# Optimization experiments

Measured on AMD Instinct MI355X. Metric: run time of the kernel, lower is better.

## Reference

```python
import jax, jax.numpy as jnp
import numpy as np

EPS = 1e-5  # BatchNorm2d default eps (eval mode with running stats)


def _bn(v, params):
    # params: [4, C] = (gamma, beta, running_mean, running_var); channel on last axis of v
    g, b, m, var = params[0], params[1], params[2], params[3]
    return (v - m) * jax.lax.rsqrt(var + EPS) * g + b


def _gather(feat, idx):
    # feat: [B, N, C], idx: [B, M, K] -> [B, M, K, C]
    B, M, K = idx.shape
    flat = jnp.take_along_axis(feat, idx.reshape(B, M * K, 1), axis=1)
    return flat.reshape(B, M, K, feat.shape[-1])


def xconv_forward(p, x, q, w1, bn1, w2, bn2, wt1, bnt1, wt2, bnt2, wt3, wc, bno):
    selu = jax.nn.selu
    B = p.shape[0]
    K = wt1.shape[2]  # kernel_size
    pT = jnp.transpose(p, (0, 2, 1))  # [B, N, 3]
    # KNN: squared distances [B, M, N], take K nearest (dilation=1)
    d2 = (jnp.sum(q * q, axis=-1, keepdims=True)
          + jnp.sum(pT * pT, axis=-1)[:, None, :]
          - 2.0 * jnp.einsum('bmc,bnc->bmn', q, pT))
    _, idx = jax.lax.top_k(-d2, K)  # [B, M, K]
    p_nb = _gather(pT, idx)                     # [B, M, K, 3]
    p_hat = p_nb - q[:, :, None, :]             # [B, M, K, 3]
    # mlp1: two 1x1 conv + BN + SELU stacks on p_hat
    h = selu(_bn(jnp.einsum('bmkc,dc->bmkd', p_hat, w1), bn1))
    h = selu(_bn(jnp.einsum('bmkd,ed->bmke', h, w2), bn2))  # [B, M, K, mid]
    # gather input features and concat
    xT = jnp.transpose(x, (0, 2, 1))            # [B, N, Cin]
    x_nb = _gather(xT, idx)                     # [B, M, K, Cin]
    x_hat = jnp.concatenate([h, x_nb], axis=-1)  # [B, M, K, mid+Cin]
    # mlp2: X-transform matrix T (conv [1,K] contracts the neighbor axis)
    t = selu(_bn(jnp.einsum('bmkc,ock->bmo', p_hat, wt1), bnt1))  # [B, M, K^2]
    t = selu(_bn(jnp.einsum('bmo,po->bmp', t, wt2), bnt2))
    t = jnp.einsum('bmp,qp->bmq', t, wt3)
    M = q.shape[1]
    T = t.reshape(B, M, K, K)                   # matches torch view(B,K,K,M).permute(0,3,1,2)
    y = jnp.matmul(T, x_hat)                    # [B, M, K, mid+Cin]
    # final conv [1,K] + BN + SELU -> [B, out, M]
    y = jnp.einsum('bmkc,ock->bmo', y, wc)
    y = selu(_bn(y, bno))
    return jnp.transpose(q, (0, 2, 1)), jnp.transpose(y, (0, 2, 1))


def _bn_pack(key, c):
    k1, k2, k3, k4 = jax.random.split(key, 4)
    gamma = 1.0 + 0.1 * jax.random.normal(k1, (c,), jnp.float32)
    beta = 0.1 * jax.random.normal(k2, (c,), jnp.float32)
    mean = 0.1 * jax.random.normal(k3, (c,), jnp.float32)
    var = jax.random.uniform(k4, (c,), jnp.float32, 0.5, 1.5)
    return jnp.stack([gamma, beta, mean, var], axis=0)


def setup_inputs() -> dict:
    B, N, M, K, CIN, COUT = 4, 8192, 2048, 16, 64, 256
    MID, K2 = COUT // 4, K * K
    key = jax.random.key(0)
    ks = jax.random.split(key, 16)
    return {
        'p': jax.random.normal(ks[0], (B, 3, N), jnp.float32),
        'x': jax.random.normal(ks[1], (B, CIN, N), jnp.float32),
        'q': jax.random.normal(ks[2], (B, M, 3), jnp.float32),
        'w1': 0.1 * jax.random.normal(ks[3], (MID, 3), jnp.float32),
        'bn1': _bn_pack(ks[4], MID),
        'w2': 0.1 * jax.random.normal(ks[5], (MID, MID), jnp.float32),
        'bn2': _bn_pack(ks[6], MID),
        'wt1': 0.1 * jax.random.normal(ks[7], (K2, 3, K), jnp.float32),
        'bnt1': _bn_pack(ks[8], K2),
        'wt2': 0.05 * jax.random.normal(ks[9], (K2, K2), jnp.float32),
        'bnt2': _bn_pack(ks[10], K2),
        'wt3': 0.05 * jax.random.normal(ks[11], (K2, K2), jnp.float32),
        'wc': 0.05 * jax.random.normal(ks[12], (COUT, MID + CIN, K), jnp.float32),
        'bno': _bn_pack(ks[13], COUT),
    }


def reference(p, x, q, w1, bn1, w2, bn2, wt1, bnt1, wt2, bnt2, wt3, wc, bno):
    return xconv_forward(p, x, q, w1, bn1, w2, bn2, wt1, bnt1, wt2, bnt2, wt3, wc, bno)
```

## Files before the change

### kernel.cpp

```cpp
#include <hip/hip_runtime.h>
#include <hip/hip_bf16.h>
#include <float.h>

#define NPTS 8192
#define KNB  16
#define CINC 64
#define MIDC 64
#define EPSBN 1e-5f

typedef unsigned short u16;
typedef u16   us8   __attribute__((ext_vector_type(8)));
typedef __bf16 bf16x8 __attribute__((ext_vector_type(8)));
typedef float  f32x4  __attribute__((ext_vector_type(4)));

__device__ __forceinline__ float selu_f(float x) {
    const float sc = 1.0507009873554805f;
    const float al = 1.6732632423543772f;
    return x > 0.f ? sc * x : sc * al * expm1f(x);
}
__device__ __forceinline__ float bn_f(float v, const float* __restrict__ bnp, int C, int c) {
    float g = bnp[c], b = bnp[C + c], mu = bnp[2 * C + c], va = bnp[3 * C + c];
    return (v - mu) * (1.0f / sqrtf(va + EPSBN)) * g + b;
}
__device__ __forceinline__ u16 f2bf(float v) {
    __hip_bfloat16 h = __float2bfloat16(v);
    return *reinterpret_cast<u16*>(&h);
}

__device__ __forceinline__ unsigned long long wavemin_u64(unsigned long long h) {
#pragma unroll
    for (int s = 32; s >= 1; s >>= 1) {
        const unsigned int ohi = __shfl_xor((unsigned int)(h >> 32), s);
        const unsigned int olo = __shfl_xor((unsigned int)(h & 0xFFFFFFFFu), s);
        const unsigned long long o = ((unsigned long long)ohi << 32) | olo;
        if (o < h) h = o;
    }
    return h;
}

__global__ __launch_bounds__(256) void knn_kernel(const float* __restrict__ p,
                                                  const float* __restrict__ q,
                                                  int* __restrict__ idx_out,
                                                  float* __restrict__ phat) {
    const int w = threadIdx.x >> 6, lane = threadIdx.x & 63;
    const int bm = blockIdx.x * 4 + w;
    const int b = bm >> 11;
    const float qx = q[bm * 3 + 0], qy = q[bm * 3 + 1], qz = q[bm * 3 + 2];
    const float qq = __fadd_rn(__fadd_rn(__fmul_rn(qx, qx), __fmul_rn(qy, qy)), __fmul_rn(qz, qz));
    const float* px = p + (size_t)b * 3 * NPTS;
    const float* py = px + NPTS;
    const float* pz = py + NPTS;

    unsigned long long mn = ~0ull;
#pragma unroll 2
    for (int j = 0; j < NPTS / 64; ++j) {
        const int n = lane + j * 64;
        const float ax = px[n], ay = py[n], az = pz[n];
        const float pp = __fadd_rn(__fadd_rn(__fmul_rn(ax, ax), __fmul_rn(ay, ay)), __fmul_rn(az, az));
        const float dt = __fmaf_rn(az, qz, __fmaf_rn(ay, qy, __fmul_rn(ax, qx)));
        const float d2 = __fsub_rn(__fadd_rn(qq, pp), __fmul_rn(2.0f, dt));
        const unsigned int bits = __float_as_uint(d2);
        const unsigned int key = bits ^ ((unsigned int)((int)bits >> 31) | 0x80000000u);
        const unsigned long long nk = ((unsigned long long)key << 32) | (unsigned int)n;
        if (nk < mn) mn = nk;
    }
    unsigned long long T;
    {
        unsigned long long mcur = mn;
        for (int r = 0; r < 16; ++r) {
            const unsigned long long h = wavemin_u64(mcur);
            if (r == 15) T = h;
            if (mcur == h) mcur = ~0ull;
        }
    }

    unsigned long long K[16];
#pragma unroll
    for (int i = 0; i < 16; ++i) K[i] = ~0ull;

#pragma unroll 2
    for (int j = 0; j < NPTS / 64; ++j) {
        const int n = lane + j * 64;
        const float ax = px[n], ay = py[n], az = pz[n];
        const float pp = __fadd_rn(__fadd_rn(__fmul_rn(ax, ax), __fmul_rn(ay, ay)), __fmul_rn(az, az));
        const float dt = __fmaf_rn(az, qz, __fmaf_rn(ay, qy, __fmul_rn(ax, qx)));
        const float d2 = __fsub_rn(__fadd_rn(qq, pp), __fmul_rn(2.0f, dt));
        const unsigned int bits = __float_as_uint(d2);
        const unsigned int key = bits ^ ((unsigned int)((int)bits >> 31) | 0x80000000u);
        const unsigned long long nk = ((unsigned long long)key << 32) | (unsigned int)n;
        if (__any(nk <= T)) {
            if (nk <= T && nk < K[15]) {
                bool c[16];
#pragma unroll
                for (int i = 0; i < 16; ++i) c[i] = nk < K[i];
#pragma unroll
                for (int i = 15; i >= 1; --i) K[i] = c[i] ? (c[i - 1] ? K[i - 1] : nk) : K[i];
                K[0] = c[0] ? nk : K[0];
            }
        }
    }

    unsigned long long win_i = 0, win_p = 0;
    for (int r = 0; r < 16; ++r) {
        const unsigned long long h = wavemin_u64(K[0]);
        const bool own = (K[0] == h);
#pragma unroll
        for (int i = 0; i < 15; ++i) K[i] = own ? K[i + 1] : K[i];
        K[15] = own ? ~0ull : K[15];
        if (r == lane) win_i = h;
        if (lane < 48 && r == (lane / 3)) win_p = h;
    }
    if (lane < 16) idx_out[bm * 16 + lane] = (int)(win_i & 0xFFFFFFFFu);
    if (lane < 48) {
        const int kk = lane / 3, c = lane - kk * 3;
        const int n = (int)(win_p & 0xFFFFFFFFu);
        phat[(size_t)bm * 48 + lane] = p[((size_t)b * 3 + c) * NPTS + n] - q[bm * 3 + c];
    }
}

__global__ __launch_bounds__(256) void mlp1_kernel(const float* __restrict__ x,
                                                   const float* __restrict__ w1,
                                                   const float* __restrict__ bn1,
                                                   const float* __restrict__ w2,
                                                   const float* __restrict__ bn2,
                                                   const int* __restrict__ idxb,
                                                   const float* __restrict__ phat,
                                                   float* __restrict__ xhat) {
    __shared__ float ph[48];
    __shared__ float h1[16 * 64];
    __shared__ float4 w2s4[16][64];
    __shared__ int idxs[16];
    const int bm = blockIdx.x;
    const int b = bm >> 11;
    const int t = threadIdx.x;
    if (t < 48) ph[t] = phat[(size_t)bm * 48 + t];
    if (t < 16) idxs[t] = idxb[bm * 16 + t];
#pragma unroll
    for (int i = 0; i < 4; ++i) {
        const int fi = t + i * 256;
        const int e = fi >> 4, dq = fi & 15;
        w2s4[dq][e] = ((const float4*)w2)[fi];
    }
    __syncthreads();
#pragma unroll
    for (int i = 0; i < 4; ++i) {
        const int o = t + i * 256;
        const int kk = o >> 6, d = o & 63;
        float s = ph[kk * 3 + 0] * w1[d * 3 + 0] + ph[kk * 3 + 1] * w1[d * 3 + 1] + ph[kk * 3 + 2] * w1[d * 3 + 2];
        h1[kk * 64 + d] = selu_f(bn_f(s, bn1, MIDC, d));
    }
    __syncthreads();
#pragma unroll
    for (int i = 0; i < 4; ++i) {
        const int o = t + i * 256;
        const int kk = o >> 6, e = o & 63;
        const float4* h4 = (const float4*)&h1[kk * 64];
        float s = 0.f;
#pragma unroll
        for (int dq = 0; dq < 16; ++dq) {
            const float4 hv = h4[dq];
            const float4 wv = w2s4[dq][e];
            s += hv.x * wv.x; s += hv.y * wv.y; s += hv.z * wv.z; s += hv.w * wv.w;
        }
        xhat[(size_t)bm * 2048 + kk * 128 + e] = selu_f(bn_f(s, bn2, MIDC, e));
    }
#pragma unroll
    for (int i = 0; i < 4; ++i) {
        const int o = t + i * 256;
        const int kk = o >> 6, c = o & 63;
        xhat[(size_t)bm * 2048 + kk * 128 + 64 + c] = x[((size_t)b * CINC + c) * NPTS + idxs[kk]];
    }
}

template <int MODE>
__global__ __launch_bounds__(256) void gemm_bt(const float* __restrict__ A, int lda,
                                               const float* __restrict__ B, int ldb,
                                               float* __restrict__ C, int ldc,
                                               int Kd, const float* __restrict__ bnp, int Nc) {
    __shared__ float As[16][68];
    __shared__ float Bs[16][68];
    const int t = threadIdx.x;
    const int tx = t & 15, ty = t >> 4;
    const int row0 = blockIdx.y * 64, col0 = blockIdx.x * 64;
    const int r = t >> 2, q4 = t & 3;
    float acc[4][4] = {};
    for (int k0 = 0; k0 < Kd; k0 += 16) {
        const float4 av = *(const float4*)(A + (size_t)(row0 + r) * lda + k0 + q4 * 4);
        const float4 bv = *(const float4*)(B + (size_t)(col0 + r) * ldb + k0 + q4 * 4);
        As[q4 * 4 + 0][r] = av.x; As[q4 * 4 + 1][r] = av.y;
        As[q4 * 4 + 2][r] = av.z; As[q4 * 4 + 3][r] = av.w;
        Bs[q4 * 4 + 0][r] = bv.x; Bs[q4 * 4 + 1][r] = bv.y;
        Bs[q4 * 4 + 2][r] = bv.z; Bs[q4 * 4 + 3][r] = bv.w;
        __syncthreads();
#pragma unroll
        for (int kk = 0; kk < 16; ++kk) {
            float a0 = As[kk][ty * 4 + 0], a1 = As[kk][ty * 4 + 1];
            float a2 = As[kk][ty * 4 + 2], a3 = As[kk][ty * 4 + 3];
            float b0 = Bs[kk][tx * 4 + 0], b1 = Bs[kk][tx * 4 + 1];
            float b2 = Bs[kk][tx * 4 + 2], b3 = Bs[kk][tx * 4 + 3];
            acc[0][0] += a0 * b0; acc[0][1] += a0 * b1; acc[0][2] += a0 * b2; acc[0][3] += a0 * b3;
            acc[1][0] += a1 * b0; acc[1][1] += a1 * b1; acc[1][2] += a1 * b2; acc[1][3] += a1 * b3;
            acc[2][0] += a2 * b0; acc[2][1] += a2 * b1; acc[2][2] += a2 * b2; acc[2][3] += a2 * b3;
            acc[3][0] += a3 * b0; acc[3][1] += a3 * b1; acc[3][2] += a3 * b2; acc[3][3] += a3 * b3;
        }
        __syncthreads();
    }
#pragma unroll
    for (int i = 0; i < 4; ++i) {
#pragma unroll
        for (int j = 0; j < 4; ++j) {
            const int row = row0 + ty * 4 + i, col = col0 + tx * 4 + j;
            float v = acc[i][j];
            if (MODE >= 1) v = selu_f(bn_f(v, bnp, Nc, col));
            if (MODE == 2) {
                C[(((size_t)(row >> 11)) * Nc + col) * 2048 + (row & 2047)] = v;
            } else {
                C[(size_t)row * ldc + col] = v;
            }
        }
    }
}

template <int EMIT_BF>
__global__ __launch_bounds__(256) void xtrans_kernel(float* __restrict__ xhat,
                                                     const float* __restrict__ tmat,
                                                     u16* __restrict__ xhb) {
    __shared__ float xs[2048];
    __shared__ float Tm[256];
    const int bm = blockIdx.x, t = threadIdx.x;
#pragma unroll
    for (int i = 0; i < 8; ++i) xs[t + i * 256] = xhat[(size_t)bm * 2048 + t + i * 256];
    Tm[t] = tmat[(size_t)bm * 256 + t];
    __syncthreads();
    float y[8];
#pragma unroll
    for (int i = 0; i < 8; ++i) {
        const int o = t + i * 256, kk = o >> 7, c = o & 127;
        float s = 0.f;
#pragma unroll
        for (int j = 0; j < 16; ++j) s += Tm[kk * 16 + j] * xs[j * 128 + c];
        y[i] = s;
    }
    if (EMIT_BF) {
#pragma unroll
        for (int i = 0; i < 8; ++i) xhb[(size_t)bm * 2048 + t + i * 256] = f2bf(y[i]);
    } else {
#pragma unroll
        for (int i = 0; i < 8; ++i) xhat[(size_t)bm * 2048 + t + i * 256] = y[i];
    }
}

__global__ __launch_bounds__(256) void gemm_mfma_final(const u16* __restrict__ XHB,
                                                       const u16* __restrict__ WCBH,
                                                       const float* __restrict__ bno,
                                                       float* __restrict__ out1) {
    __shared__ u16 As[64][72];
    __shared__ u16 Bs[64][72];
    const int t = threadIdx.x;
    const int w = t >> 6, lane = t & 63;
    const int wm = w >> 1, wn = w & 1;
    const int row0 = blockIdx.y * 64, col0 = blockIdx.x * 64;
    const int srow = t >> 2, skq = t & 3;

    f32x4 acc[2][2] = {};

    for (int k0 = 0; k0 < 2048; k0 += 64) {
        __syncthreads();
        const u16* ga = XHB + (size_t)(row0 + srow) * 2048 + k0 + skq * 16;
        const u16* gb = WCBH + (size_t)(col0 + srow) * 2048 + k0 + skq * 16;
        *(us8*)&As[srow][skq * 16 + 0] = *(const us8*)(ga + 0);
        *(us8*)&As[srow][skq * 16 + 8] = *(const us8*)(ga + 8);
        *(us8*)&Bs[srow][skq * 16 + 0] = *(const us8*)(gb + 0);
        *(us8*)&Bs[srow][skq * 16 + 8] = *(const us8*)(gb + 8);
        __syncthreads();
#pragma unroll
        for (int ks = 0; ks < 2; ++ks) {
            const int kb = ks * 32 + (lane >> 4) * 8;
            const bf16x8 a0 = *(const bf16x8*)&As[wm * 32 + (lane & 15)][kb];
            const bf16x8 a1 = *(const bf16x8*)&As[wm * 32 + 16 + (lane & 15)][kb];
            const bf16x8 b0 = *(const bf16x8*)&Bs[wn * 32 + (lane & 15)][kb];
            const bf16x8 b1 = *(const bf16x8*)&Bs[wn * 32 + 16 + (lane & 15)][kb];
            acc[0][0] = __builtin_amdgcn_mfma_f32_16x16x32_bf16(a0, b0, acc[0][0], 0, 0, 0);
            acc[0][1] = __builtin_amdgcn_mfma_f32_16x16x32_bf16(a0, b1, acc[0][1], 0, 0, 0);
            acc[1][0] = __builtin_amdgcn_mfma_f32_16x16x32_bf16(a1, b0, acc[1][0], 0, 0, 0);
            acc[1][1] = __builtin_amdgcn_mfma_f32_16x16x32_bf16(a1, b1, acc[1][1], 0, 0, 0);
        }
    }
#pragma unroll
    for (int mi = 0; mi < 2; ++mi) {
#pragma unroll
        for (int ni = 0; ni < 2; ++ni) {
            const int col = col0 + wn * 32 + ni * 16 + (lane & 15);
            const int rowg = row0 + wm * 32 + mi * 16 + (lane >> 4) * 4;
            const int b = rowg >> 11, m = rowg & 2047;
            float4 v;
            v.x = selu_f(bn_f(acc[mi][ni][0], bno, 256, col));
            v.y = selu_f(bn_f(acc[mi][ni][1], bno, 256, col));
            v.z = selu_f(bn_f(acc[mi][ni][2], bno, 256, col));
            v.w = selu_f(bn_f(acc[mi][ni][3], bno, 256, col));
            *(float4*)(out1 + ((size_t)(b * 256 + col)) * 2048 + m) = v;
        }
    }
}

__global__ void transpose_q_kernel(const float* __restrict__ q, float* __restrict__ out0) {
    const int t = blockIdx.x * 256 + threadIdx.x;
    if (t >= 4 * 3 * 2048) return;
    const int b = t / 6144, rem = t % 6144, c = rem >> 11, m = rem & 2047;
    out0[t] = q[((size_t)b * 2048 + m) * 3 + c];
}
__global__ void prep_wt1_kernel(const float* __restrict__ wt1, float* __restrict__ wt1r) {
    const int t = blockIdx.x * 256 + threadIdx.x;
    if (t >= 256 * 48) return;
    const int o = t / 48, rem = t % 48, kk = rem / 3, c = rem % 3;
    wt1r[t] = wt1[o * 48 + c * 16 + kk];
}
__global__ void prep_wc_kernel(const float* __restrict__ wc, float* __restrict__ wcb) {
    const int t = blockIdx.x * 256 + threadIdx.x;
    if (t >= 256 * 2048) return;
    const int o = t >> 11, f = t & 2047, kk = f >> 7, c = f & 127;
    wcb[t] = wc[o * 2048 + c * 16 + kk];
}
__global__ void prep_wcbh_kernel(const float* __restrict__ wcb, u16* __restrict__ wcbh) {
    const int t = blockIdx.x * 256 + threadIdx.x;
    if (t >= 256 * 2048) return;
    wcbh[t] = f2bf(wcb[t]);
}

extern "C" void kernel_launch(void* const* d_in, const int* in_sizes, int n_in,
                              void* d_out, int out_size, void* d_ws, size_t ws_size,
                              hipStream_t stream) {
    const float* p    = (const float*)d_in[0];
    const float* x    = (const float*)d_in[1];
    const float* q    = (const float*)d_in[2];
    const float* w1   = (const float*)d_in[3];
    const float* bn1  = (const float*)d_in[4];
    const float* w2   = (const float*)d_in[5];
    const float* bn2  = (const float*)d_in[6];
    const float* wt1  = (const float*)d_in[7];
    const float* bnt1 = (const float*)d_in[8];
    const float* wt2  = (const float*)d_in[9];
    const float* bnt2 = (const float*)d_in[10];
    const float* wt3  = (const float*)d_in[11];
    const float* wc   = (const float*)d_in[12];
    const float* bno  = (const float*)d_in[13];
    float* out = (float*)d_out;

    float* ws   = (float*)d_ws;
    float* WT1R = ws;
    float* WCB  = WT1R + 12288;
    int*   IDX  = (int*)(WCB + 524288);
    float* PHAT = (float*)(IDX + 131072);
    float* BUFA = PHAT + 393216;
    float* BUFB = BUFA + 2097152;
    float* XHAT = BUFB + 2097152;
    u16*   XHB  = (u16*)(XHAT + 16777216);
    u16*   WCBH = XHB + 16777216;
    const size_t NEED = (22032384ull + 8388608ull + 262144ull) * 4ull;
    const bool use_mfma = (ws_size >= NEED);

    transpose_q_kernel<<<96, 256, 0, stream>>>(q, out);
    prep_wt1_kernel<<<48, 256, 0, stream>>>(wt1, WT1R);
    prep_wc_kernel<<<2048, 256, 0, stream>>>(wc, WCB);
    if (use_mfma) prep_wcbh_kernel<<<2048, 256, 0, stream>>>(WCB, WCBH);

    knn_kernel<<<2048, 256, 0, stream>>>(p, q, IDX, PHAT);
    mlp1_kernel<<<8192, 256, 0, stream>>>(x, w1, bn1, w2, bn2, IDX, PHAT, XHAT);

    gemm_bt<1><<<dim3(4, 128), 256, 0, stream>>>(PHAT, 48, WT1R, 48, BUFA, 256, 48, bnt1, 256);
    gemm_bt<1><<<dim3(4, 128), 256, 0, stream>>>(BUFA, 256, wt2, 256, BUFB, 256, 256, bnt2, 256);
    gemm_bt<0><<<dim3(4, 128), 256, 0, stream>>>(BUFB, 256, wt3, 256, BUFA, 256, 256, nullptr, 256);

    if (use_mfma) {
        xtrans_kernel<1><<<8192, 256, 0, stream>>>(XHAT, BUFA, XHB);
        gemm_mfma_final<<<dim3(4, 128), 256, 0, stream>>>(XHB, WCBH, bno, out + 24576);
    } else {
        xtrans_kernel<0><<<8192, 256, 0, stream>>>(XHAT, BUFA, nullptr);
        gemm_bt<2><<<dim3(4, 128), 256, 0, stream>>>(XHAT, 2048, WCB, 2048, out + 24576, 0, 2048, bno, 256);
    }
}
```

Before: 292.4 us.

## Pre-transpose x to point-major and vectorize neighbor gather and X-transform

Adds a tiled transpose kernel that writes x as [B,N,C] into scratch (reusing BUFA before the T-matrix GEMMs overwrite it). The mlp1 neighbor gather then reads contiguous float4 rows per neighbor instead of 64 strided scalar loads, which removes uncoalesced gathers. The xtrans kernel is also reworked to load and store float4/ushort4 and to compute four channels per thread. The cost is one extra kernel launch plus a full read and write of x.

After: 295.5 us. No clear change (+1.0%).

```diff
diff --git a/kernel.cpp b/kernel.cpp
--- a/kernel.cpp
+++ b/kernel.cpp
@@ -118,7 +118,27 @@
     }
 }
 
-__global__ __launch_bounds__(256) void mlp1_kernel(const float* __restrict__ x,
+__global__ __launch_bounds__(256) void transpose_x_kernel(const float* __restrict__ x,
+                                                          float* __restrict__ xT) {
+    __shared__ float tile[64][65];
+    const int b = blockIdx.y;
+    const int n0 = blockIdx.x * 64;
+    const int t = threadIdx.x;
+    const int tn = t & 63, tq = t >> 6;
+#pragma unroll
+    for (int i = 0; i < 16; ++i) {
+        const int c = tq * 16 + i;
+        tile[c][tn] = x[((size_t)b * 64 + c) * NPTS + n0 + tn];
+    }
+    __syncthreads();
+#pragma unroll
+    for (int i = 0; i < 16; ++i) {
+        const int n = tq * 16 + i;
+        xT[((size_t)b * NPTS + n0 + n) * 64 + tn] = tile[tn][n];
+    }
+}
+
+__global__ __launch_bounds__(256) void mlp1_kernel(const float* __restrict__ xT,
                                                    const float* __restrict__ w1,
                                                    const float* __restrict__ bn1,
                                                    const float* __restrict__ w2,
@@ -164,11 +184,10 @@
         }
         xhat[(size_t)bm * 2048 + kk * 128 + e] = selu_f(bn_f(s, bn2, MIDC, e));
     }
-#pragma unroll
-    for (int i = 0; i < 4; ++i) {
-        const int o = t + i * 256;
-        const int kk = o >> 6, c = o & 63;
-        xhat[(size_t)bm * 2048 + kk * 128 + 64 + c] = x[((size_t)b * CINC + c) * NPTS + idxs[kk]];
+    {
+        const int kk = t >> 4, c4 = t & 15;
+        const float4 v = *(const float4*)(xT + ((size_t)b * NPTS + idxs[kk]) * 64 + c4 * 4);
+        *(float4*)(xhat + (size_t)bm * 2048 + kk * 128 + 64 + c4 * 4) = v;
     }
 }
 
@@ -225,28 +244,37 @@
 __global__ __launch_bounds__(256) void xtrans_kernel(float* __restrict__ xhat,
                                                      const float* __restrict__ tmat,
                                                      u16* __restrict__ xhb) {
-    __shared__ float xs[2048];
+    __shared__ float4 xs4[16][32];
     __shared__ float Tm[256];
     const int bm = blockIdx.x, t = threadIdx.x;
 #pragma unroll
-    for (int i = 0; i < 8; ++i) xs[t + i * 256] = xhat[(size_t)bm * 2048 + t + i * 256];
+    for (int i = 0; i < 2; ++i) {
+        const int f4 = t + i * 256;
+        const int j = f4 >> 5, c4 = f4 & 31;
+        xs4[j][c4] = ((const float4*)(xhat + (size_t)bm * 2048))[f4];
+    }
     Tm[t] = tmat[(size_t)bm * 256 + t];
     __syncthreads();
-    float y[8];
-#pragma unroll
-    for (int i = 0; i < 8; ++i) {
-        const int o = t + i * 256, kk = o >> 7, c = o & 127;
-        float s = 0.f;
-#pragma unroll
-        for (int j = 0; j < 16; ++j) s += Tm[kk * 16 + j] * xs[j * 128 + c];
-        y[i] = s;
-    }
-    if (EMIT_BF) {
-#pragma unroll
-        for (int i = 0; i < 8; ++i) xhb[(size_t)bm * 2048 + t + i * 256] = f2bf(y[i]);
-    } else {
-#pragma unroll
-        for (int i = 0; i < 8; ++i) xhat[(size_t)bm * 2048 + t + i * 256] = y[i];
+    const int c4 = t & 31, kk0 = t >> 5;
+#pragma unroll
+    for (int half = 0; half < 2; ++half) {
+        const int kk = kk0 + half * 8;
+        float sx = 0.f, sy = 0.f, sz = 0.f, sw = 0.f;
+#pragma unroll
+        for (int j = 0; j < 16; ++j) {
+            const float tv = Tm[kk * 16 + j];
+            const float4 xv = xs4[j][c4];
+            sx += tv * xv.x; sy += tv * xv.y; sz += tv * xv.z; sw += tv * xv.w;
+        }
+        const size_t base = (size_t)bm * 2048 + kk * 128 + c4 * 4;
+        if (EMIT_BF) {
+            ushort4 o;
+            o.x = f2bf(sx); o.y = f2bf(sy); o.z = f2bf(sz); o.w = f2bf(sw);
+            *(ushort4*)(xhb + base) = o;
+        } else {
+            float4 o; o.x = sx; o.y = sy; o.z = sz; o.w = sw;
+            *(float4*)(xhat + base) = o;
+        }
     }
 }
 
@@ -356,6 +384,7 @@
     float* XHAT = BUFB + 2097152;
     u16*   XHB  = (u16*)(XHAT + 16777216);
     u16*   WCBH = XHB + 16777216;
+    float* XT   = BUFA;
     const size_t NEED = (22032384ull + 8388608ull + 262144ull) * 4ull;
     const bool use_mfma = (ws_size >= NEED);
 
@@ -363,9 +392,10 @@
     prep_wt1_kernel<<<48, 256, 0, stream>>>(wt1, WT1R);
     prep_wc_kernel<<<2048, 256, 0, stream>>>(wc, WCB);
     if (use_mfma) prep_wcbh_kernel<<<2048, 256, 0, stream>>>(WCB, WCBH);
+    transpose_x_kernel<<<dim3(128, 4), 256, 0, stream>>>(x, XT);
 
     knn_kernel<<<2048, 256, 0, stream>>>(p, q, IDX, PHAT);
-    mlp1_kernel<<<8192, 256, 0, stream>>>(x, w1, bn1, w2, bn2, IDX, PHAT, XHAT);
+    mlp1_kernel<<<8192, 256, 0, stream>>>(XT, w1, bn1, w2, bn2, IDX, PHAT, XHAT);
 
     gemm_bt<1><<<dim3(4, 128), 256, 0, stream>>>(PHAT, 48, WT1R, 48, BUFA, 256, 48, bnt1, 256);
     gemm_bt<1><<<dim3(4, 128), 256, 0, stream>>>(BUFA, 256, wt2, 256, BUFB, 256, 256, bnt2, 256);
```
